# Performance work log

Hardware: AMD Instinct MI355X
Metric: run time of the kernel (lower is better)

Reference implementation:

```python
import jax, jax.numpy as jnp
import numpy as np

OUT_F, IN_F = 8192, 4096
TOKENS = 512


def _unpack_int2_to_ternary(packed, alpha, dtype):
    # packed: [out_f, in_f//4] ints 0..255; 4 two-bit codes per byte.
    # code 0 -> -1, code 2 -> +1, codes 1/3 -> 0; then scale by per-row alpha.
    shifts = jnp.arange(4, dtype=packed.dtype) * 2  # [0,2,4,6]
    two_bit = (packed[:, :, None] >> shifts[None, None, :]) & 3  # [out_f, in_f//4, 4]
    two_bit = two_bit.reshape(packed.shape[0], -1)  # [out_f, in_f]
    sign = jnp.where(two_bit == 2, 1.0, jnp.where(two_bit == 0, -1.0, 0.0)).astype(dtype)
    return sign * alpha.astype(dtype)[:, None]


def setup_inputs() -> dict:
    key = jax.random.key(0)
    k1, k2, k3, k4 = jax.random.split(key, 4)
    x = jax.random.normal(k1, (TOKENS, IN_F), dtype=jnp.float32)
    weight_int2 = jax.random.randint(k2, (OUT_F, IN_F // 4), 0, 256, dtype=jnp.int32)
    alpha = jax.random.uniform(k3, (OUT_F,), dtype=jnp.float32, minval=0.01, maxval=0.05)
    bias = jax.random.normal(k4, (OUT_F,), dtype=jnp.float32) * 0.01
    return {"x": x, "weight_int2": weight_int2, "alpha": alpha, "bias": bias}


def reference(x, weight_int2, alpha, bias):
    W = _unpack_int2_to_ternary(weight_int2, alpha, x.dtype)  # [out_f, in_f]
    out = x @ W.T  # [tokens, out_f]
    return out + bias
```

## Files before the change

kernel.cpp:

```cpp
#include <hip/hip_runtime.h>
#include <hip/hip_bf16.h>

typedef unsigned int u32;
typedef unsigned short u16;

#define TOKENS 512
#define OUT_F  8192
#define IN_F   4096
#define KPACK  (IN_F / 4)
#define TMB 128
#define TNB 128
#define BKW 128
#define NWIN (IN_F / BKW)

typedef __attribute__((ext_vector_type(8))) short bf16x8;
typedef __attribute__((ext_vector_type(4))) float f32x4;
typedef __attribute__((ext_vector_type(16))) float f32x16;

__device__ __forceinline__ u32 pack_bf16x2(float a, float b) {
    __hip_bfloat162 h = __float22bfloat162_rn(make_float2(a, b));
    union { __hip_bfloat162 h2; u32 u; } cvt;
    cvt.h2 = h;
    return cvt.u;
}

__device__ __forceinline__ u32 decode_pair(u32 d) {
    u32 s = (__umul24(d, 0x808202u) & 0x06060606u) + 0x01000100u;
    return __builtin_amdgcn_perm(0x00003F80u, 0x0000BF80u, s);
}
__device__ __forceinline__ bf16x8 decode_frag(u32 w, int sh) {
    union { bf16x8 v; u32 u[4]; } c;
    c.u[0] = decode_pair((w >> (sh + 0)) & 0xFu);
    c.u[1] = decode_pair((w >> (sh + 4)) & 0xFu);
    c.u[2] = decode_pair((w >> (sh + 8)) & 0xFu);
    c.u[3] = decode_pair((w >> (sh + 12)) & 0xFu);
    return c.v;
}

__device__ __forceinline__ void async_ld16(const void* g, void* l) {
    __builtin_amdgcn_global_load_lds(
        (const __attribute__((address_space(1))) u32*)g,
        (__attribute__((address_space(3))) u32*)l, 16, 0, 0);
}

__global__ __launch_bounds__(256) void convert_x(const float* __restrict__ X,
                                                 u16* __restrict__ Xb) {
    int i = (blockIdx.x * 256 + threadIdx.x) * 8;
    float4 a = *(const float4*)(X + i);
    float4 b = *(const float4*)(X + i + 4);
    uint4 q;
    q.x = pack_bf16x2(a.x, a.y);
    q.y = pack_bf16x2(a.z, a.w);
    q.z = pack_bf16x2(b.x, b.y);
    q.w = pack_bf16x2(b.z, b.w);
    *(uint4*)(Xb + i) = q;
}

__global__ __launch_bounds__(256) void repack_w7(const u32* __restrict__ W2,
                                                 uint2* __restrict__ W7) {
    __shared__ u32 dense[128 * 32];
    const int ngrp = blockIdx.x;
    const int kc   = blockIdx.y;
    const int t = threadIdx.x;
#pragma unroll
    for (int i = 0; i < 16; ++i) {
        int id = t + 256 * i;
        int col = id >> 5, jq = id & 31;
        uint4 wv = *(const uint4*)(W2 + (size_t)(ngrp * 128 + col) * KPACK + kc * 128 + jq * 4);
        dense[col * 32 + (jq ^ (col & 31))] =
            (wv.x & 0xFFu) | ((wv.y & 0xFFu) << 8) | ((wv.z & 0xFFu) << 16) | ((wv.w & 0xFFu) << 24);
    }
    __syncthreads();
    const u16* sp = (const u16*)dense;
#pragma unroll
    for (int p = 0; p < 8; ++p) {
        int e = t + 256 * p;
        int lane = e & 63;
        int kq = (e >> 6) & 3;
        int wloc = (e >> 8) & 3;
        int nh = (e >> 10) & 1;
        int h = lane >> 5;
        int c0 = nh * 64 + (lane & 31), c1 = c0 + 32;
        int j0 = wloc * 8 + kq * 2;
        u32 x0 = sp[((c0 * 32 + (j0 ^ (c0 & 31))) << 1) | h];
        u32 x1 = sp[((c0 * 32 + ((j0 + 1) ^ (c0 & 31))) << 1) | h];
        u32 y0 = sp[((c1 * 32 + (j0 ^ (c1 & 31))) << 1) | h];
        u32 y1 = sp[((c1 * 32 + ((j0 + 1) ^ (c1 & 31))) << 1) | h];
        uint2 o;
        o.x = x0 | (x1 << 16);
        o.y = y0 | (y1 << 16);
        int w = kc * 4 + wloc;
        W7[(((size_t)(ngrp * 2 + nh) * 32 + w) * 4 + kq) * 64 + lane] = o;
    }
}

__global__ __launch_bounds__(512, 2) void ternary_gemm8(
    const u16* __restrict__ Xb,
    const uint2* __restrict__ W7,
    const float* __restrict__ alpha,
    const float* __restrict__ bias,
    float* __restrict__ Out)
{
    __shared__ u16 As[2][TMB * BKW];

    const int tid  = threadIdx.x;
    const int lane = tid & 63;
    const int wave = tid >> 6;
    const int kq = wave & 3;
    const int nh = wave >> 2;

    const int m0 = blockIdx.x * TMB;
    const int ngrp = blockIdx.y;
    const int n0 = ngrp * TNB;

    f32x16 acc[4][2];
#pragma unroll
    for (int mt = 0; mt < 4; ++mt)
#pragma unroll
        for (int nt = 0; nt < 2; ++nt)
#pragma unroll
            for (int i = 0; i < 16; ++i)
                acc[mt][nt][i] = 0.f;

    const u16* ga[4];
    u32 lbase[4];
#pragma unroll
    for (int i = 0; i < 4; ++i) {
        int rbase = wave * 16 + i * 4;
        int row = rbase + (lane >> 4);
        int cd = (lane & 15) ^ (row & 15);
        ga[i] = Xb + (size_t)(m0 + row) * IN_F + cd * 8;
        lbase[i] = rbase * BKW;
    }

    int ofsA[4][2];
#pragma unroll
    for (int mt = 0; mt < 4; ++mt)
#pragma unroll
        for (int ks = 0; ks < 2; ++ks) {
            int row = mt * 32 + (lane & 31);
            int chunk = kq * 4 + ks * 2 + (lane >> 5);
            ofsA[mt][ks] = row * BKW + ((chunk ^ (row & 15))) * 8;
        }

    const uint2* wp = W7 + ((size_t)(ngrp * 2 + nh) * NWIN * 4 + kq) * 64 + lane;

    uint2 wcur = wp[0];
    uint2 wnext = wp[256];
#pragma unroll
    for (int i = 0; i < 4; ++i) async_ld16(ga[i], &As[0][lbase[i]]);
    __syncthreads();

    for (int w = 0; w < NWIN; ++w) {
        const int buf = w & 1;
        if (w + 1 < NWIN) {
            const int koff = (w + 1) * BKW;
#pragma unroll
            for (int i = 0; i < 4; ++i)
                async_ld16(ga[i] + koff, &As[buf ^ 1][lbase[i]]);
        }
        uint2 wnn = make_uint2(0, 0);
        if (w + 2 < NWIN) wnn = wp[(size_t)(w + 2) * 256];

        const u16* ab = As[buf];
#pragma unroll
        for (int ks = 0; ks < 2; ++ks) {
            bf16x8 a0 = *(const bf16x8*)(ab + ofsA[0][ks]);
            bf16x8 a1 = *(const bf16x8*)(ab + ofsA[1][ks]);
            bf16x8 a2 = *(const bf16x8*)(ab + ofsA[2][ks]);
            bf16x8 a3 = *(const bf16x8*)(ab + ofsA[3][ks]);
            bf16x8 b0 = decode_frag(wcur.x, ks * 16);
            bf16x8 b1 = decode_frag(wcur.y, ks * 16);
            acc[0][0] = __builtin_amdgcn_mfma_f32_32x32x16_bf16(a0, b0, acc[0][0], 0, 0, 0);
            acc[1][0] = __builtin_amdgcn_mfma_f32_32x32x16_bf16(a1, b0, acc[1][0], 0, 0, 0);
            acc[2][0] = __builtin_amdgcn_mfma_f32_32x32x16_bf16(a2, b0, acc[2][0], 0, 0, 0);
            acc[3][0] = __builtin_amdgcn_mfma_f32_32x32x16_bf16(a3, b0, acc[3][0], 0, 0, 0);
            acc[0][1] = __builtin_amdgcn_mfma_f32_32x32x16_bf16(a0, b1, acc[0][1], 0, 0, 0);
            acc[1][1] = __builtin_amdgcn_mfma_f32_32x32x16_bf16(a1, b1, acc[1][1], 0, 0, 0);
            acc[2][1] = __builtin_amdgcn_mfma_f32_32x32x16_bf16(a2, b1, acc[2][1], 0, 0, 0);
            acc[3][1] = __builtin_amdgcn_mfma_f32_32x32x16_bf16(a3, b1, acc[3][1], 0, 0, 0);
        }
        wcur = wnext;
        wnext = wnn;
        __syncthreads();
    }

    f32x4* red = (f32x4*)As;
#pragma unroll 1
    for (int q = 1; q < 4; ++q) {
        if (kq == q) {
            f32x4* dst = red + nh * 2048 + lane;
#pragma unroll
            for (int mt = 0; mt < 4; ++mt)
#pragma unroll
                for (int nt = 0; nt < 2; ++nt)
#pragma unroll
                    for (int sub = 0; sub < 4; ++sub) {
                        f32x4 v = {acc[mt][nt][sub * 4 + 0], acc[mt][nt][sub * 4 + 1],
                                   acc[mt][nt][sub * 4 + 2], acc[mt][nt][sub * 4 + 3]};
                        dst[(mt * 8 + nt * 4 + sub) * 64] = v;
                    }
        }
        __syncthreads();
        if (kq == 0) {
            const f32x4* src = red + nh * 2048 + lane;
#pragma unroll
            for (int mt = 0; mt < 4; ++mt)
#pragma unroll
                for (int nt = 0; nt < 2; ++nt)
#pragma unroll
                    for (int sub = 0; sub < 4; ++sub) {
                        f32x4 v = src[(mt * 8 + nt * 4 + sub) * 64];
#pragma unroll
                        for (int i = 0; i < 4; ++i)
                            acc[mt][nt][sub * 4 + i] += v[i];
                    }
        }
        __syncthreads();
    }

    if (kq == 0) {
#pragma unroll
        for (int nt = 0; nt < 2; ++nt) {
            int ncol = n0 + nh * 64 + nt * 32 + (lane & 31);
            float av = alpha[ncol];
            float bv = bias[ncol];
#pragma unroll
            for (int mt = 0; mt < 4; ++mt) {
#pragma unroll
                for (int r = 0; r < 16; ++r) {
                    int row = m0 + mt * 32 + (r & 3) + 8 * (r >> 2) + 4 * (lane >> 5);
                    Out[(size_t)row * OUT_F + ncol] = acc[mt][nt][r] * av + bv;
                }
            }
        }
    }
}

__global__ void ternary_naive(const float* __restrict__ X, const u32* __restrict__ W2,
                              const float* __restrict__ alpha, const float* __restrict__ bias,
                              float* __restrict__ Out) {
    int o  = blockIdx.x * 64 + (threadIdx.x & 63);
    int tk = blockIdx.y * 4 + (threadIdx.x >> 6);
    const float* x = X + (size_t)tk * IN_F;
    const u32* w = W2 + (size_t)o * KPACK;
    float s = 0.f;
    for (int d = 0; d < KPACK; ++d) {
        u32 b = w[d] & 0xFFu;
        const float* xp = x + d * 4;
#pragma unroll
        for (int j = 0; j < 4; ++j) {
            u32 c = (b >> (2 * j)) & 3u;
            float wv = (c == 2u) ? 1.f : ((c == 0u) ? -1.f : 0.f);
            s += xp[j] * wv;
        }
    }
    Out[(size_t)tk * OUT_F + o] = s * alpha[o] + bias[o];
}

extern "C" void kernel_launch(void* const* d_in, const int* in_sizes, int n_in,
                              void* d_out, int out_size, void* d_ws, size_t ws_size,
                              hipStream_t stream) {
    const float* x = (const float*)d_in[0];
    const u32* w2 = (const u32*)d_in[1];
    const float* alpha = (const float*)d_in[2];
    const float* bias  = (const float*)d_in[3];
    float* out = (float*)d_out;

    const size_t xb_bytes = (size_t)TOKENS * IN_F * sizeof(u16);
    const size_t w7_bytes = (size_t)OUT_F * IN_F / 4;

    if (ws_size >= xb_bytes + w7_bytes) {
        u16* xb = (u16*)d_ws;
        uint2* w7 = (uint2*)((char*)d_ws + xb_bytes);
        convert_x<<<(TOKENS * IN_F) / (256 * 8), 256, 0, stream>>>(x, xb);
        repack_w7<<<dim3(64, 8), 256, 0, stream>>>(w2, w7);
        ternary_gemm8<<<dim3(TOKENS / TMB, OUT_F / TNB), 512, 0, stream>>>(xb, w7, alpha, bias, out);
    } else {
        ternary_naive<<<dim3(OUT_F / 64, TOKENS / 4), 256, 0, stream>>>(x, w2, alpha, bias, out);
    }
}
```

Baseline: 129.7 us.

## Pre-swizzle activations into MFMA fragment layout and load directly to registers

The x conversion is merged into the weight repack kernel, and it now writes bf16 activations in a per-wave MFMA fragment order. The GEMM kernel then loads A fragments straight from global memory into registers, double-buffered across even and odd windows. This removes the LDS staging buffer and the per-window __syncthreads. Block indices are also remapped to group M and N tiles for cache locality, and one launch is saved. The cost is more register pressure from holding 16 uint4 A fragments per thread, plus redundant global A reads across N-groups that now go through L2 instead of being shared in LDS.

```diff
diff --git a/kernel.cpp b/kernel.cpp
--- a/kernel.cpp
+++ b/kernel.cpp
@@ -37,31 +37,39 @@
     return c.v;
 }
 
-__device__ __forceinline__ void async_ld16(const void* g, void* l) {
-    __builtin_amdgcn_global_load_lds(
-        (const __attribute__((address_space(1))) u32*)g,
-        (__attribute__((address_space(3))) u32*)l, 16, 0, 0);
-}
-
-__global__ __launch_bounds__(256) void convert_x(const float* __restrict__ X,
-                                                 u16* __restrict__ Xb) {
-    int i = (blockIdx.x * 256 + threadIdx.x) * 8;
-    float4 a = *(const float4*)(X + i);
-    float4 b = *(const float4*)(X + i + 4);
-    uint4 q;
-    q.x = pack_bf16x2(a.x, a.y);
-    q.y = pack_bf16x2(a.z, a.w);
-    q.z = pack_bf16x2(b.x, b.y);
-    q.w = pack_bf16x2(b.z, b.w);
-    *(uint4*)(Xb + i) = q;
-}
-
-__global__ __launch_bounds__(256) void repack_w7(const u32* __restrict__ W2,
-                                                 uint2* __restrict__ W7) {
+__global__ __launch_bounds__(256) void prep(const float* __restrict__ X,
+                                            uint4* __restrict__ Xa,
+                                            const u32* __restrict__ W2,
+                                            uint2* __restrict__ W7) {
     __shared__ u32 dense[128 * 32];
+    const int t = threadIdx.x;
+
+    if (blockIdx.y == 8) {
+        int base = blockIdx.x * 32768 + t * 8;
+#pragma unroll
+        for (int r = 0; r < 16; ++r) {
+            int i = base + r * 2048;
+            float4 a = *(const float4*)(X + i);
+            float4 b = *(const float4*)(X + i + 4);
+            uint4 q;
+            q.x = pack_bf16x2(a.x, a.y);
+            q.y = pack_bf16x2(a.z, a.w);
+            q.z = pack_bf16x2(b.x, b.y);
+            q.w = pack_bf16x2(b.z, b.w);
+            int row = i >> 12;
+            int k0  = i & 4095;
+            int mblk = row >> 7, mt = (row >> 5) & 3, lr = row & 31;
+            int w = k0 >> 7, kq = (k0 >> 5) & 3, ks = (k0 >> 4) & 1;
+            int half = (k0 >> 3) & 1;
+            int lane = half * 32 + lr;
+            int slot = ks * 4 + mt;
+            Xa[(((size_t)(mblk * 4 + kq) * NWIN + w) * 8 + slot) * 64 + lane] = q;
+        }
+        return;
+    }
+
     const int ngrp = blockIdx.x;
     const int kc   = blockIdx.y;
-    const int t = threadIdx.x;
 #pragma unroll
     for (int i = 0; i < 16; ++i) {
         int id = t + 256 * i;
@@ -94,14 +102,14 @@
     }
 }
 
-__global__ __launch_bounds__(512, 2) void ternary_gemm8(
-    const u16* __restrict__ Xb,
+__global__ __launch_bounds__(512, 2) void ternary_gemm17(
+    const uint4* __restrict__ Xa,
     const uint2* __restrict__ W7,
     const float* __restrict__ alpha,
     const float* __restrict__ bias,
     float* __restrict__ Out)
 {
-    __shared__ u16 As[2][TMB * BKW];
+    __shared__ f32x4 red[4096];
 
     const int tid  = threadIdx.x;
     const int lane = tid & 63;
@@ -109,8 +117,11 @@
     const int kq = wave & 3;
     const int nh = wave >> 2;
 
-    const int m0 = blockIdx.x * TMB;
-    const int ngrp = blockIdx.y;
+    const int bid = blockIdx.x;
+    const int k8 = bid & 7;
+    const int mblk = k8 >> 1;
+    const int ngrp = (k8 & 1) * 32 + (bid >> 3);
+    const int m0 = mblk * TMB;
     const int n0 = ngrp * TNB;
 
     f32x16 acc[4][2];
@@ -122,70 +133,57 @@
             for (int i = 0; i < 16; ++i)
                 acc[mt][nt][i] = 0.f;
 
-    const u16* ga[4];
-    u32 lbase[4];
-#pragma unroll
-    for (int i = 0; i < 4; ++i) {
-        int rbase = wave * 16 + i * 4;
-        int row = rbase + (lane >> 4);
-        int cd = (lane & 15) ^ (row & 15);
-        ga[i] = Xb + (size_t)(m0 + row) * IN_F + cd * 8;
-        lbase[i] = rbase * BKW;
-    }
-
-    int ofsA[4][2];
-#pragma unroll
-    for (int mt = 0; mt < 4; ++mt)
+    const uint4* ap0 = Xa + (((size_t)(mblk * 4 + kq) * NWIN) * 8) * 64 + lane;
+    const uint2* wp = W7 + ((size_t)(ngrp * 2 + nh) * NWIN * 4 + kq) * 64 + lane;
+
+    uint4 aE[8], aO[8];
+    uint2 bE, bO;
+
+    auto loadA = [&](int w, uint4 (&dst)[8]) {
+        const uint4* p = ap0 + (size_t)w * 512;
+#pragma unroll
+        for (int s = 0; s < 8; ++s)
+            dst[s] = p[s * 64];
+    };
+
+    auto window_compute = [&](const uint4 (&a)[8], uint2 bq) {
 #pragma unroll
         for (int ks = 0; ks < 2; ++ks) {
-            int row = mt * 32 + (lane & 31);
-            int chunk = kq * 4 + ks * 2 + (lane >> 5);
-            ofsA[mt][ks] = row * BKW + ((chunk ^ (row & 15))) * 8;
-        }
-
-    const uint2* wp = W7 + ((size_t)(ngrp * 2 + nh) * NWIN * 4 + kq) * 64 + lane;
-
-    uint2 wcur = wp[0];
-    uint2 wnext = wp[256];
-#pragma unroll
-    for (int i = 0; i < 4; ++i) async_ld16(ga[i], &As[0][lbase[i]]);
-    __syncthreads();
-
-    for (int w = 0; w < NWIN; ++w) {
-        const int buf = w & 1;
-        if (w + 1 < NWIN) {
-            const int koff = (w + 1) * BKW;
-#pragma unroll
-            for (int i = 0; i < 4; ++i)
-                async_ld16(ga[i] + koff, &As[buf ^ 1][lbase[i]]);
-        }
-        uint2 wnn = make_uint2(0, 0);
-        if (w + 2 < NWIN) wnn = wp[(size_t)(w + 2) * 256];
-
-        const u16* ab = As[buf];
-#pragma unroll
-        for (int ks = 0; ks < 2; ++ks) {
-            bf16x8 a0 = *(const bf16x8*)(ab + ofsA[0][ks]);
-            bf16x8 a1 = *(const bf16x8*)(ab + ofsA[1][ks]);
-            bf16x8 a2 = *(const bf16x8*)(ab + ofsA[2][ks]);
-            bf16x8 a3 = *(const bf16x8*)(ab + ofsA[3][ks]);
-            bf16x8 b0 = decode_frag(wcur.x, ks * 16);
-            bf16x8 b1 = decode_frag(wcur.y, ks * 16);
-            acc[0][0] = __builtin_amdgcn_mfma_f32_32x32x16_bf16(a0, b0, acc[0][0], 0, 0, 0);
-            acc[1][0] = __builtin_amdgcn_mfma_f32_32x32x16_bf16(a1, b0, acc[1][0], 0, 0, 0);
-            acc[2][0] = __builtin_amdgcn_mfma_f32_32x32x16_bf16(a2, b0, acc[2][0], 0, 0, 0);
-            acc[3][0] = __builtin_amdgcn_mfma_f32_32x32x16_bf16(a3, b0, acc[3][0], 0, 0, 0);
-            acc[0][1] = __builtin_amdgcn_mfma_f32_32x32x16_bf16(a0, b1, acc[0][1], 0, 0, 0);
-            acc[1][1] = __builtin_amdgcn_mfma_f32_32x32x16_bf16(a1, b1, acc[1][1], 0, 0, 0);
-            acc[2][1] = __builtin_amdgcn_mfma_f32_32x32x16_bf16(a2, b1, acc[2][1], 0, 0, 0);
-            acc[3][1] = __builtin_amdgcn_mfma_f32_32x32x16_bf16(a3, b1, acc[3][1], 0, 0, 0);
-        }
-        wcur = wnext;
-        wnext = wnn;
-        __syncthreads();
-    }
-
-    f32x4* red = (f32x4*)As;
+            union { uint4 q; bf16x8 v; } a0, a1, a2, a3;
+            a0.q = a[ks * 4 + 0];
+            a1.q = a[ks * 4 + 1];
+            a2.q = a[ks * 4 + 2];
+            a3.q = a[ks * 4 + 3];
+            bf16x8 b0 = decode_frag(bq.x, ks * 16);
+            bf16x8 b1 = decode_frag(bq.y, ks * 16);
+            acc[0][0] = __builtin_amdgcn_mfma_f32_32x32x16_bf16(a0.v, b0, acc[0][0], 0, 0, 0);
+            acc[1][0] = __builtin_amdgcn_mfma_f32_32x32x16_bf16(a1.v, b0, acc[1][0], 0, 0, 0);
+            acc[2][0] = __builtin_amdgcn_mfma_f32_32x32x16_bf16(a2.v, b0, acc[2][0], 0, 0, 0);
+            acc[3][0] = __builtin_amdgcn_mfma_f32_32x32x16_bf16(a3.v, b0, acc[3][0], 0, 0, 0);
+            acc[0][1] = __builtin_amdgcn_mfma_f32_32x32x16_bf16(a0.v, b1, acc[0][1], 0, 0, 0);
+            acc[1][1] = __builtin_amdgcn_mfma_f32_32x32x16_bf16(a1.v, b1, acc[1][1], 0, 0, 0);
+            acc[2][1] = __builtin_amdgcn_mfma_f32_32x32x16_bf16(a2.v, b1, acc[2][1], 0, 0, 0);
+            acc[3][1] = __builtin_amdgcn_mfma_f32_32x32x16_bf16(a3.v, b1, acc[3][1], 0, 0, 0);
+        }
+    };
+
+    loadA(0, aE);
+    bE = wp[0];
+#pragma unroll 1
+    for (int p = 0; p < NWIN / 2 - 1; ++p) {
+        const int w = 2 * p;
+        loadA(w + 1, aO);
+        bO = wp[(size_t)(w + 1) * 256];
+        window_compute(aE, bE);
+        loadA(w + 2, aE);
+        bE = wp[(size_t)(w + 2) * 256];
+        window_compute(aO, bO);
+    }
+    loadA(31, aO);
+    bO = wp[(size_t)31 * 256];
+    window_compute(aE, bE);
+    window_compute(aO, bO);
+
 #pragma unroll 1
     for (int q = 1; q < 4; ++q) {
         if (kq == q) {
@@ -267,15 +265,14 @@
     const float* bias  = (const float*)d_in[3];
     float* out = (float*)d_out;
 
-    const size_t xb_bytes = (size_t)TOKENS * IN_F * sizeof(u16);
+    const size_t xa_bytes = (size_t)TOKENS * IN_F * sizeof(u16);
     const size_t w7_bytes = (size_t)OUT_F * IN_F / 4;
 
-    if (ws_size >= xb_bytes + w7_bytes) {
-        u16* xb = (u16*)d_ws;
-        uint2* w7 = (uint2*)((char*)d_ws + xb_bytes);
-        convert_x<<<(TOKENS * IN_F) / (256 * 8), 256, 0, stream>>>(x, xb);
-        repack_w7<<<dim3(64, 8), 256, 0, stream>>>(w2, w7);
-        ternary_gemm8<<<dim3(TOKENS / TMB, OUT_F / TNB), 512, 0, stream>>>(xb, w7, alpha, bias, out);
+    if (ws_size >= xa_bytes + w7_bytes) {
+        uint4* xa = (uint4*)d_ws;
+        uint2* w7 = (uint2*)((char*)d_ws + xa_bytes);
+        prep<<<dim3(64, 9), 256, 0, stream>>>(x, xa, w2, w7);
+        ternary_gemm17<<<256, 512, 0, stream>>>(xa, w7, alpha, bias, out);
     } else {
         ternary_naive<<<dim3(OUT_F / 64, TOKENS / 4), 256, 0, stream>>>(x, w2, alpha, bias, out);
     }
```

After: 137.6 us. 1.06x slower.
